# Optimization experiments

Hardware: AMD Instinct MI355X
Metric: run time of the kernel (lower is better)

Reference implementation:

```python
import jax, jax.numpy as jnp
import numpy as np

D_MODEL = 512
N_HEAD = 8
HEAD_DIM = D_MODEL // N_HEAD
B, T = 8, 384
N_TOKENS = 2048


def setup_inputs() -> dict:
    key = jax.random.key(0)
    ks = jax.random.split(key, 16)
    w_scale = 1.0 / np.sqrt(D_MODEL)
    inp = {
        "x": jax.random.normal(ks[0], (N_TOKENS, D_MODEL), jnp.float32),
        "relkeys": jax.random.normal(ks[1], (B, T, T, HEAD_DIM), jnp.float32),
        "relvals": jax.random.normal(ks[2], (B, T, T, HEAD_DIM), jnp.float32),
        "Wq": jax.random.normal(ks[3], (D_MODEL, D_MODEL), jnp.float32) * w_scale,
        "bq": jnp.zeros((D_MODEL,), jnp.float32),
        "Wk": jax.random.normal(ks[4], (D_MODEL, D_MODEL), jnp.float32) * w_scale,
        "bk": jnp.zeros((D_MODEL,), jnp.float32),
        "Wv": jax.random.normal(ks[5], (D_MODEL, D_MODEL), jnp.float32) * w_scale,
        "bv": jnp.zeros((D_MODEL,), jnp.float32),
        "Wp": jax.random.normal(ks[6], (D_MODEL, D_MODEL), jnp.float32) * w_scale,
        "bp": jnp.zeros((D_MODEL,), jnp.float32),
        "padpack_index": jax.random.randint(ks[7], (B, T), 0, N_TOKENS, jnp.int32),
        "padpack_batch": jnp.sort(jax.random.randint(ks[8], (B, T), 0, 40, jnp.int32), axis=-1),
        "padpack_inverse_index": jax.random.randint(ks[9], (N_TOKENS,), 0, B * T, jnp.int32),
    }
    return inp


def reference(x, relkeys, relvals, Wq, bq, Wk, bk, Wv, bv, Wp, bp,
              padpack_index, padpack_batch, padpack_inverse_index):
    C = D_MODEL
    scale = 1.0 / np.sqrt(HEAD_DIM).astype(np.float32)
    # gather ragged tokens into dense padded-packed layout [B,T,C]
    xp = x[padpack_index]

    def heads(W, b):
        # torch nn.Linear: x @ W.T + b ; -> [B,H,T,Dh]
        return (xp @ W.T + b).reshape(B, T, N_HEAD, HEAD_DIM).transpose(0, 2, 1, 3)

    q, k, v = heads(Wq, bq), heads(Wk, bk), heads(Wv, bv)

    att = jnp.einsum('bhsd,bhtd->bhst', q, k) * scale
    att = att + jnp.einsum('bhsd,bstd->bhst', q, relkeys) * scale
    # block-diagonal mask: slots from different ragged sequences can't attend
    mask = (padpack_batch[:, :, None] != padpack_batch[:, None, :])[:, None]  # [B,1,T,T]
    att = jnp.where(mask, jnp.float32(-1e9), att)
    att = jax.nn.softmax(att, axis=-1)

    y = jnp.einsum('bhst,bhtd->bhsd', att, v)
    y = y + jnp.einsum('bhst,bstd->bhsd', att, relvals)
    y = y.transpose(0, 2, 1, 3).reshape(B, T, C)
    y = y @ Wp.T + bp
    # scatter back to ragged token order via inverse index
    return y.reshape(B * T, C)[padpack_inverse_index]
```

## Files before the change

### kernel.cpp

```cpp
#include <hip/hip_runtime.h>

using short8  = __attribute__((ext_vector_type(8))) short;
using floatx4 = __attribute__((ext_vector_type(4))) float;

#define D_MODEL 512
#define N_HEAD 8
#define HEAD_DIM 64
#define B_ 8
#define T_ 384
#define N_SLOTS 3072
#define N_TOK 2048

__device__ __forceinline__ float bf2f(ushort u) {
  union { uint u32; float f; } c; c.u32 = ((uint)u) << 16; return c.f;
}
__device__ __forceinline__ float2 bf2x2(uint u) {
  union { uint u32; float f; } lo, hi;
  lo.u32 = u << 16; hi.u32 = u & 0xffff0000u;
  float2 r; r.x = lo.f; r.y = hi.f; return r;
}
__device__ __forceinline__ ushort f2bf(float f) {
  union { float f; uint u; } c; c.f = f;
  uint x = c.u;
  x += 0x7fffu + ((x >> 16) & 1u);
  return (ushort)(x >> 16);
}

__global__ __launch_bounds__(256) void probe_dtype(const ushort* __restrict__ x,
                                                   int* __restrict__ flag) {
  __shared__ int cnt;
  if (threadIdx.x == 0) cnt = 0;
  __syncthreads();
  int c = 0;
  for (int i = threadIdx.x; i < 1024; i += 256) {
    ushort w = x[2 * i];
    int e = (w >> 7) & 0xFF;
    if (e >= 100 && e <= 160) c++;
  }
  atomicAdd(&cnt, c);
  __syncthreads();
  if (threadIdx.x == 0) flag[0] = (cnt < 700) ? 1 : 0;
}

__device__ __forceinline__ void load8(const void* p, size_t off, int isF32, float* av) {
  if (isF32) {
    const float* fp = (const float*)p + off;
    float4 a = *(const float4*)fp;
    float4 b = *(const float4*)(fp + 4);
    av[0]=a.x; av[1]=a.y; av[2]=a.z; av[3]=a.w;
    av[4]=b.x; av[5]=b.y; av[6]=b.z; av[7]=b.w;
  } else {
    const ushort* up = (const ushort*)p + off;
    uint4 w = *(const uint4*)up;
    float2 p0 = bf2x2(w.x), p1 = bf2x2(w.y), p2 = bf2x2(w.z), p3 = bf2x2(w.w);
    av[0]=p0.x; av[1]=p0.y; av[2]=p1.x; av[3]=p1.y;
    av[4]=p2.x; av[5]=p2.y; av[6]=p3.x; av[7]=p3.y;
  }
}

__device__ __forceinline__ void pack_hl(const float* av, uint4& ph, uint4& pl) {
  ushort hh[8], ll[8];
  #pragma unroll
  for (int j = 0; j < 8; j++) {
    hh[j] = f2bf(av[j]);
    ll[j] = f2bf(av[j] - bf2f(hh[j]));
  }
  ph.x = (uint)hh[0] | ((uint)hh[1] << 16);
  ph.y = (uint)hh[2] | ((uint)hh[3] << 16);
  ph.z = (uint)hh[4] | ((uint)hh[5] << 16);
  ph.w = (uint)hh[6] | ((uint)hh[7] << 16);
  pl.x = (uint)ll[0] | ((uint)ll[1] << 16);
  pl.y = (uint)ll[2] | ((uint)ll[3] << 16);
  pl.z = (uint)ll[4] | ((uint)ll[5] << 16);
  pl.w = (uint)ll[6] | ((uint)ll[7] << 16);
}

template<int A_WS, int MODE>
__global__ __launch_bounds__(256) void gemm_bt(
    const void* __restrict__ Av, const int* __restrict__ gidx,
    const void* __restrict__ Wv, const void* __restrict__ biasv,
    void* __restrict__ outv, const int* __restrict__ flag)
{
  const int f32m = flag[0];
  __shared__ __align__(16) ushort Ash[64][40], Asl[64][40];
  __shared__ __align__(16) ushort Bsh[64][40], Bsl[64][40];
  const int m0 = blockIdx.x * 64;
  const int n0 = blockIdx.y * 64;
  const int tid = threadIdx.x;
  const int wave = tid >> 6, lane = tid & 63;
  const int quad = lane >> 4, l16 = lane & 15;
  const int srow = tid >> 2, sseg = tid & 3;

  const int arow = m0 + srow;
  const int atok = gidx[arow];
  const int brow = n0 + srow;

  floatx4 acc[4];
  #pragma unroll
  for (int i = 0; i < 4; i++) acc[i] = (floatx4){0.f, 0.f, 0.f, 0.f};

  for (int k0 = 0; k0 < D_MODEL; k0 += 32) {
    float av[8];
    uint4 ph, pl;
    load8(Av, (size_t)atok * D_MODEL + k0 + sseg * 8, A_WS ? 1 : f32m, av);
    pack_hl(av, ph, pl);
    *(uint4*)&Ash[srow][sseg * 8] = ph;
    *(uint4*)&Asl[srow][sseg * 8] = pl;
    load8(Wv, (size_t)brow * D_MODEL + k0 + sseg * 8, f32m, av);
    pack_hl(av, ph, pl);
    *(uint4*)&Bsh[srow][sseg * 8] = ph;
    *(uint4*)&Bsl[srow][sseg * 8] = pl;
    __syncthreads();

    short8 ah = *(const short8*)&Ash[wave * 16 + l16][quad * 8];
    short8 al = *(const short8*)&Asl[wave * 16 + l16][quad * 8];
    #pragma unroll
    for (int cg = 0; cg < 4; cg++) {
      short8 bh = *(const short8*)&Bsh[cg * 16 + l16][quad * 8];
      short8 bl = *(const short8*)&Bsl[cg * 16 + l16][quad * 8];
      acc[cg] = __builtin_amdgcn_mfma_f32_16x16x32_bf16(ah, bh, acc[cg], 0, 0, 0);
      acc[cg] = __builtin_amdgcn_mfma_f32_16x16x32_bf16(ah, bl, acc[cg], 0, 0, 0);
      acc[cg] = __builtin_amdgcn_mfma_f32_16x16x32_bf16(al, bh, acc[cg], 0, 0, 0);
    }
    __syncthreads();
  }

  #pragma unroll
  for (int cg = 0; cg < 4; cg++) {
    const int col = n0 + cg * 16 + l16;
    const float bv = f32m ? ((const float*)biasv)[col] : bf2f(((const ushort*)biasv)[col]);
    #pragma unroll
    for (int r = 0; r < 4; r++) {
      const int row = m0 + wave * 16 + quad * 4 + r;
      const float val = acc[cg][r] + bv;
      if (MODE == 0) {
        const int bb = row / T_;
        const int t = row - bb * T_;
        const int hh = col >> 6;
        const int dh = col & 63;
        ((float*)outv)[(((size_t)(bb * N_HEAD + hh) * T_ + t) * HEAD_DIM) + dh] = val;
      } else {
        if (f32m) ((float*)outv)[(size_t)row * D_MODEL + col] = val;
        else      ((ushort*)outv)[(size_t)row * D_MODEL + col] = f2bf(val);
      }
    }
  }
}

__global__ __launch_bounds__(256) void attn_kernel(
    const float* __restrict__ q, const float* __restrict__ k,
    const float* __restrict__ v, const void* __restrict__ rkv,
    const void* __restrict__ rvv, const int* __restrict__ batch,
    float* __restrict__ y, const int* __restrict__ flag)
{
  const int f32m = flag[0];
  const int s = blockIdx.x;
  const int b = blockIdx.y;
  const int tid = threadIdx.x;

  __shared__ float qf[N_HEAD][HEAD_DIM];
  __shared__ float probs[N_HEAD][T_];
  __shared__ int   bt[T_];
  __shared__ float rsum[N_HEAD];

  for (int i = tid; i < D_MODEL; i += 256) {
    const int h = i >> 6, d = i & 63;
    qf[h][d] = q[(((size_t)(b * N_HEAD + h) * T_ + s) * HEAD_DIM) + d];
  }
  for (int i = tid; i < T_; i += 256) bt[i] = batch[b * T_ + i];
  __syncthreads();

  const int myb = bt[s];
  const int h = tid >> 5, tl = tid & 31;
  const float scale = 0.125f;

  const float* kbase = k + ((size_t)(b * N_HEAD + h) * T_) * HEAD_DIM;
  const size_t roff = ((size_t)(b * T_ + s)) * T_ * HEAD_DIM;

  float sc[12];
  #pragma unroll
  for (int i = 0; i < 12; i++) {
    const int t = i * 32 + tl;
    const float4* kp = (const float4*)(kbase + (size_t)t * HEAD_DIM);
    float acc = 0.f;
    if (f32m) {
      const float4* rp = (const float4*)((const float*)rkv + roff + (size_t)t * HEAD_DIM);
      #pragma unroll
      for (int c = 0; c < 16; c++) {
        const float4 kw = kp[c];
        const float4 rw = rp[c];
        const float4 qa = *(const float4*)&qf[h][c * 4];
        acc = fmaf(qa.x, kw.x + rw.x, acc);
        acc = fmaf(qa.y, kw.y + rw.y, acc);
        acc = fmaf(qa.z, kw.z + rw.z, acc);
        acc = fmaf(qa.w, kw.w + rw.w, acc);
      }
    } else {
      const uint4* rp = (const uint4*)((const ushort*)rkv + roff + (size_t)t * HEAD_DIM);
      #pragma unroll
      for (int c = 0; c < 8; c++) {
        const uint4 rw = rp[c];
        const float4 k0 = kp[2 * c];
        const float4 k1 = kp[2 * c + 1];
        const float4 qa = *(const float4*)&qf[h][c * 8];
        const float4 qb = *(const float4*)&qf[h][c * 8 + 4];
        const float2 r0 = bf2x2(rw.x), r1 = bf2x2(rw.y);
        const float2 r2 = bf2x2(rw.z), r3 = bf2x2(rw.w);
        acc = fmaf(qa.x, k0.x + r0.x, acc);
        acc = fmaf(qa.y, k0.y + r0.y, acc);
        acc = fmaf(qa.z, k0.z + r1.x, acc);
        acc = fmaf(qa.w, k0.w + r1.y, acc);
        acc = fmaf(qb.x, k1.x + r2.x, acc);
        acc = fmaf(qb.y, k1.y + r2.y, acc);
        acc = fmaf(qb.z, k1.z + r3.x, acc);
        acc = fmaf(qb.w, k1.w + r3.y, acc);
      }
    }
    sc[i] = (bt[t] == myb) ? acc * scale : -1e9f;
  }

  float m = sc[0];
  #pragma unroll
  for (int i = 1; i < 12; i++) m = fmaxf(m, sc[i]);
  #pragma unroll
  for (int off = 1; off < 32; off <<= 1) m = fmaxf(m, __shfl_xor(m, off, 64));
  float sum = 0.f;
  #pragma unroll
  for (int i = 0; i < 12; i++) { sc[i] = __expf(sc[i] - m); sum += sc[i]; }
  #pragma unroll
  for (int off = 1; off < 32; off <<= 1) sum += __shfl_xor(sum, off, 64);
  #pragma unroll
  for (int i = 0; i < 12; i++) probs[h][i * 32 + tl] = sc[i];
  if (tl == 0) rsum[h] = 1.f / sum;
  __syncthreads();

  const int d0 = tl * 2;
  const float* vp = v + ((size_t)(b * N_HEAD + h) * T_) * HEAD_DIM + d0;
  float ax = 0.f, ay = 0.f;
  if (f32m) {
    const float* rvp = (const float*)rvv + roff + d0;
    #pragma unroll 4
    for (int t = 0; t < T_; t++) {
      const float p = probs[h][t];
      const float2 vv = *(const float2*)(vp + (size_t)t * HEAD_DIM);
      const float2 rr = *(const float2*)(rvp + (size_t)t * HEAD_DIM);
      ax = fmaf(p, vv.x + rr.x, ax);
      ay = fmaf(p, vv.y + rr.y, ay);
    }
  } else {
    const ushort* rvp = (const ushort*)rvv + roff + d0;
    #pragma unroll 4
    for (int t = 0; t < T_; t++) {
      const float p = probs[h][t];
      const float2 vv = *(const float2*)(vp + (size_t)t * HEAD_DIM);
      const float2 rr = bf2x2(*(const uint*)(rvp + (size_t)t * HEAD_DIM));
      ax = fmaf(p, vv.x + rr.x, ax);
      ay = fmaf(p, vv.y + rr.y, ay);
    }
  }
  const float rs = rsum[h];
  float2 o; o.x = ax * rs; o.y = ay * rs;
  *(float2*)(y + ((size_t)(b * T_ + s)) * D_MODEL + h * HEAD_DIM + d0) = o;
}

extern "C" void kernel_launch(void* const* d_in, const int* in_sizes, int n_in,
                              void* d_out, int out_size, void* d_ws, size_t ws_size,
                              hipStream_t stream) {
  const void* x    = d_in[0];
  const void* relk = d_in[1];
  const void* relv = d_in[2];
  const void* Wq   = d_in[3];
  const void* bq   = d_in[4];
  const void* Wk   = d_in[5];
  const void* bk   = d_in[6];
  const void* Wv   = d_in[7];
  const void* bv   = d_in[8];
  const void* Wp   = d_in[9];
  const void* bp   = d_in[10];
  const int* pidx   = (const int*)d_in[11];
  const int* pbatch = (const int*)d_in[12];
  const int* pinv   = (const int*)d_in[13];

  float* ws = (float*)d_ws;
  const size_t SE = (size_t)N_SLOTS * D_MODEL;
  float* qb = ws;
  float* kb = ws + SE;
  float* vb = ws + 2 * SE;
  float* yb = ws + 3 * SE;
  int* flag = (int*)((char*)d_ws + 28u * 1024u * 1024u);

  probe_dtype<<<1, 256, 0, stream>>>((const ushort*)x, flag);
  gemm_bt<0, 0><<<dim3(48, 8), 256, 0, stream>>>(x, pidx, Wq, bq, qb, flag);
  gemm_bt<0, 0><<<dim3(48, 8), 256, 0, stream>>>(x, pidx, Wk, bk, kb, flag);
  gemm_bt<0, 0><<<dim3(48, 8), 256, 0, stream>>>(x, pidx, Wv, bv, vb, flag);
  attn_kernel<<<dim3(T_, B_), 256, 0, stream>>>(qb, kb, vb, relk, relv, pbatch, yb, flag);
  gemm_bt<1, 1><<<dim3(32, 8), 256, 0, stream>>>(yb, pinv, Wp, bp, d_out, flag);
}
```

Baseline: 1.369 ms.

## Prefetch GEMM tiles into registers and widen attention loads with more ILP

The projection GEMM now loads the next k-slice from global memory into registers while the current slice is multiplied, so load latency overlaps MFMA work. The attention score loop is split into a helper with four independent accumulators and processes two key rows per iteration to expose more memory-level parallelism. The PV loop is remapped so each thread handles 8 contiguous dims over a quarter of the key range with float4 loads, followed by a cross-lane shuffle reduction. A launch bound of 4 blocks per CU is added, which may constrain registers given the larger per-thread state.

```diff
diff --git a/kernel.cpp b/kernel.cpp
--- a/kernel.cpp
+++ b/kernel.cpp
@@ -99,18 +99,25 @@
   #pragma unroll
   for (int i = 0; i < 4; i++) acc[i] = (floatx4){0.f, 0.f, 0.f, 0.f};
 
+  float avA[8], avB[8];
+  load8(Av, (size_t)atok * D_MODEL + sseg * 8, A_WS ? 1 : f32m, avA);
+  load8(Wv, (size_t)brow * D_MODEL + sseg * 8, f32m, avB);
+
   for (int k0 = 0; k0 < D_MODEL; k0 += 32) {
-    float av[8];
     uint4 ph, pl;
-    load8(Av, (size_t)atok * D_MODEL + k0 + sseg * 8, A_WS ? 1 : f32m, av);
-    pack_hl(av, ph, pl);
+    pack_hl(avA, ph, pl);
     *(uint4*)&Ash[srow][sseg * 8] = ph;
     *(uint4*)&Asl[srow][sseg * 8] = pl;
-    load8(Wv, (size_t)brow * D_MODEL + k0 + sseg * 8, f32m, av);
-    pack_hl(av, ph, pl);
+    pack_hl(avB, ph, pl);
     *(uint4*)&Bsh[srow][sseg * 8] = ph;
     *(uint4*)&Bsl[srow][sseg * 8] = pl;
     __syncthreads();
+
+    float nvA[8], nvB[8];
+    if (k0 + 32 < D_MODEL) {
+      load8(Av, (size_t)atok * D_MODEL + k0 + 32 + sseg * 8, A_WS ? 1 : f32m, nvA);
+      load8(Wv, (size_t)brow * D_MODEL + k0 + 32 + sseg * 8, f32m, nvB);
+    }
 
     short8 ah = *(const short8*)&Ash[wave * 16 + l16][quad * 8];
     short8 al = *(const short8*)&Asl[wave * 16 + l16][quad * 8];
@@ -123,6 +130,9 @@
       acc[cg] = __builtin_amdgcn_mfma_f32_16x16x32_bf16(al, bh, acc[cg], 0, 0, 0);
     }
     __syncthreads();
+
+    #pragma unroll
+    for (int j = 0; j < 8; j++) { avA[j] = nvA[j]; avB[j] = nvB[j]; }
   }
 
   #pragma unroll
@@ -147,7 +157,61 @@
   }
 }
 
-__global__ __launch_bounds__(256) void attn_kernel(
+__device__ __forceinline__ float dot64(const float* kb, const void* rv, size_t ro,
+                                       int f32m, const float* qrow) {
+  float a0 = 0.f, a1 = 0.f, a2 = 0.f, a3 = 0.f;
+  const float4* kp = (const float4*)kb;
+  if (f32m) {
+    const float4* rp = (const float4*)((const float*)rv + ro);
+    #pragma unroll
+    for (int c = 0; c < 16; c += 4) {
+      const float4 k0 = kp[c],   r0 = rp[c];
+      const float4 k1 = kp[c+1], r1 = rp[c+1];
+      const float4 k2 = kp[c+2], r2 = rp[c+2];
+      const float4 k3 = kp[c+3], r3 = rp[c+3];
+      const float4 q0 = *(const float4*)(qrow + c * 4);
+      const float4 q1 = *(const float4*)(qrow + c * 4 + 4);
+      const float4 q2 = *(const float4*)(qrow + c * 4 + 8);
+      const float4 q3 = *(const float4*)(qrow + c * 4 + 12);
+      a0 = fmaf(q0.x, k0.x + r0.x, a0); a0 = fmaf(q0.y, k0.y + r0.y, a0);
+      a0 = fmaf(q0.z, k0.z + r0.z, a0); a0 = fmaf(q0.w, k0.w + r0.w, a0);
+      a1 = fmaf(q1.x, k1.x + r1.x, a1); a1 = fmaf(q1.y, k1.y + r1.y, a1);
+      a1 = fmaf(q1.z, k1.z + r1.z, a1); a1 = fmaf(q1.w, k1.w + r1.w, a1);
+      a2 = fmaf(q2.x, k2.x + r2.x, a2); a2 = fmaf(q2.y, k2.y + r2.y, a2);
+      a2 = fmaf(q2.z, k2.z + r2.z, a2); a2 = fmaf(q2.w, k2.w + r2.w, a2);
+      a3 = fmaf(q3.x, k3.x + r3.x, a3); a3 = fmaf(q3.y, k3.y + r3.y, a3);
+      a3 = fmaf(q3.z, k3.z + r3.z, a3); a3 = fmaf(q3.w, k3.w + r3.w, a3);
+    }
+  } else {
+    const uint4* rp = (const uint4*)((const ushort*)rv + ro);
+    #pragma unroll
+    for (int c = 0; c < 8; c += 2) {
+      const uint4 rwa = rp[c];
+      const uint4 rwb = rp[c + 1];
+      const float4 k0 = kp[2*c],   k1 = kp[2*c+1];
+      const float4 k2 = kp[2*c+2], k3 = kp[2*c+3];
+      const float4 q0 = *(const float4*)(qrow + c * 8);
+      const float4 q1 = *(const float4*)(qrow + c * 8 + 4);
+      const float4 q2 = *(const float4*)(qrow + c * 8 + 8);
+      const float4 q3 = *(const float4*)(qrow + c * 8 + 12);
+      const float2 r0 = bf2x2(rwa.x), r1 = bf2x2(rwa.y);
+      const float2 r2 = bf2x2(rwa.z), r3 = bf2x2(rwa.w);
+      const float2 r4 = bf2x2(rwb.x), r5 = bf2x2(rwb.y);
+      const float2 r6 = bf2x2(rwb.z), r7 = bf2x2(rwb.w);
+      a0 = fmaf(q0.x, k0.x + r0.x, a0); a0 = fmaf(q0.y, k0.y + r0.y, a0);
+      a0 = fmaf(q0.z, k0.z + r1.x, a0); a0 = fmaf(q0.w, k0.w + r1.y, a0);
+      a1 = fmaf(q1.x, k1.x + r2.x, a1); a1 = fmaf(q1.y, k1.y + r2.y, a1);
+      a1 = fmaf(q1.z, k1.z + r3.x, a1); a1 = fmaf(q1.w, k1.w + r3.y, a1);
+      a2 = fmaf(q2.x, k2.x + r4.x, a2); a2 = fmaf(q2.y, k2.y + r4.y, a2);
+      a2 = fmaf(q2.z, k2.z + r5.x, a2); a2 = fmaf(q2.w, k2.w + r5.y, a2);
+      a3 = fmaf(q3.x, k3.x + r6.x, a3); a3 = fmaf(q3.y, k3.y + r6.y, a3);
+      a3 = fmaf(q3.z, k3.z + r7.x, a3); a3 = fmaf(q3.w, k3.w + r7.y, a3);
+    }
+  }
+  return (a0 + a1) + (a2 + a3);
+}
+
+__global__ __launch_bounds__(256, 4) void attn_kernel(
     const float* __restrict__ q, const float* __restrict__ k,
     const float* __restrict__ v, const void* __restrict__ rkv,
     const void* __restrict__ rvv, const int* __restrict__ batch,
@@ -158,8 +222,8 @@
   const int b = blockIdx.y;
   const int tid = threadIdx.x;
 
-  __shared__ float qf[N_HEAD][HEAD_DIM];
-  __shared__ float probs[N_HEAD][T_];
+  __shared__ __align__(16) float qf[N_HEAD][HEAD_DIM];
+  __shared__ __align__(16) float probs[N_HEAD][T_];
   __shared__ int   bt[T_];
   __shared__ float rsum[N_HEAD];
 
@@ -179,44 +243,15 @@
 
   float sc[12];
   #pragma unroll
-  for (int i = 0; i < 12; i++) {
-    const int t = i * 32 + tl;
-    const float4* kp = (const float4*)(kbase + (size_t)t * HEAD_DIM);
-    float acc = 0.f;
-    if (f32m) {
-      const float4* rp = (const float4*)((const float*)rkv + roff + (size_t)t * HEAD_DIM);
-      #pragma unroll
-      for (int c = 0; c < 16; c++) {
-        const float4 kw = kp[c];
-        const float4 rw = rp[c];
-        const float4 qa = *(const float4*)&qf[h][c * 4];
-        acc = fmaf(qa.x, kw.x + rw.x, acc);
-        acc = fmaf(qa.y, kw.y + rw.y, acc);
-        acc = fmaf(qa.z, kw.z + rw.z, acc);
-        acc = fmaf(qa.w, kw.w + rw.w, acc);
-      }
-    } else {
-      const uint4* rp = (const uint4*)((const ushort*)rkv + roff + (size_t)t * HEAD_DIM);
-      #pragma unroll
-      for (int c = 0; c < 8; c++) {
-        const uint4 rw = rp[c];
-        const float4 k0 = kp[2 * c];
-        const float4 k1 = kp[2 * c + 1];
-        const float4 qa = *(const float4*)&qf[h][c * 8];
-        const float4 qb = *(const float4*)&qf[h][c * 8 + 4];
-        const float2 r0 = bf2x2(rw.x), r1 = bf2x2(rw.y);
-        const float2 r2 = bf2x2(rw.z), r3 = bf2x2(rw.w);
-        acc = fmaf(qa.x, k0.x + r0.x, acc);
-        acc = fmaf(qa.y, k0.y + r0.y, acc);
-        acc = fmaf(qa.z, k0.z + r1.x, acc);
-        acc = fmaf(qa.w, k0.w + r1.y, acc);
-        acc = fmaf(qb.x, k1.x + r2.x, acc);
-        acc = fmaf(qb.y, k1.y + r2.y, acc);
-        acc = fmaf(qb.z, k1.z + r3.x, acc);
-        acc = fmaf(qb.w, k1.w + r3.y, acc);
-      }
-    }
-    sc[i] = (bt[t] == myb) ? acc * scale : -1e9f;
+  for (int i = 0; i < 6; i++) {
+    const int ta = i * 32 + tl;
+    const int tb = ta + 192;
+    const float sa = dot64(kbase + (size_t)ta * HEAD_DIM, rkv,
+                           roff + (size_t)ta * HEAD_DIM, f32m, &qf[h][0]);
+    const float sb = dot64(kbase + (size_t)tb * HEAD_DIM, rkv,
+                           roff + (size_t)tb * HEAD_DIM, f32m, &qf[h][0]);
+    sc[i]     = (bt[ta] == myb) ? sa * scale : -1e9f;
+    sc[i + 6] = (bt[tb] == myb) ? sb * scale : -1e9f;
   }
 
   float m = sc[0];
@@ -230,37 +265,76 @@
   #pragma unroll
   for (int off = 1; off < 32; off <<= 1) sum += __shfl_xor(sum, off, 64);
   #pragma unroll
-  for (int i = 0; i < 12; i++) probs[h][i * 32 + tl] = sc[i];
+  for (int i = 0; i < 6; i++) {
+    probs[h][i * 32 + tl]       = sc[i];
+    probs[h][(i + 6) * 32 + tl] = sc[i + 6];
+  }
   if (tl == 0) rsum[h] = 1.f / sum;
   __syncthreads();
 
-  const int d0 = tl * 2;
+  const int dq = tl & 7, tq = tl >> 3;
+  const int d0 = dq * 8;
+  const int t0 = tq * 96;
   const float* vp = v + ((size_t)(b * N_HEAD + h) * T_) * HEAD_DIM + d0;
-  float ax = 0.f, ay = 0.f;
+
+  float ac[8];
+  #pragma unroll
+  for (int j = 0; j < 8; j++) ac[j] = 0.f;
+
   if (f32m) {
     const float* rvp = (const float*)rvv + roff + d0;
     #pragma unroll 4
-    for (int t = 0; t < T_; t++) {
+    for (int t = t0; t < t0 + 96; t++) {
       const float p = probs[h][t];
-      const float2 vv = *(const float2*)(vp + (size_t)t * HEAD_DIM);
-      const float2 rr = *(const float2*)(rvp + (size_t)t * HEAD_DIM);
-      ax = fmaf(p, vv.x + rr.x, ax);
-      ay = fmaf(p, vv.y + rr.y, ay);
+      const float4 v0 = *(const float4*)(vp + (size_t)t * HEAD_DIM);
+      const float4 v1 = *(const float4*)(vp + (size_t)t * HEAD_DIM + 4);
+      const float4 r0 = *(const float4*)(rvp + (size_t)t * HEAD_DIM);
+      const float4 r1 = *(const float4*)(rvp + (size_t)t * HEAD_DIM + 4);
+      ac[0] = fmaf(p, v0.x + r0.x, ac[0]);
+      ac[1] = fmaf(p, v0.y + r0.y, ac[1]);
+      ac[2] = fmaf(p, v0.z + r0.z, ac[2]);
+      ac[3] = fmaf(p, v0.w + r0.w, ac[3]);
+      ac[4] = fmaf(p, v1.x + r1.x, ac[4]);
+      ac[5] = fmaf(p, v1.y + r1.y, ac[5]);
+      ac[6] = fmaf(p, v1.z + r1.z, ac[6]);
+      ac[7] = fmaf(p, v1.w + r1.w, ac[7]);
     }
   } else {
     const ushort* rvp = (const ushort*)rvv + roff + d0;
     #pragma unroll 4
-    for (int t = 0; t < T_; t++) {
+    for (int t = t0; t < t0 + 96; t++) {
       const float p = probs[h][t];
-      const float2 vv = *(const float2*)(vp + (size_t)t * HEAD_DIM);
-      const float2 rr = bf2x2(*(const uint*)(rvp + (size_t)t * HEAD_DIM));
-      ax = fmaf(p, vv.x + rr.x, ax);
-      ay = fmaf(p, vv.y + rr.y, ay);
-    }
-  }
-  const float rs = rsum[h];
-  float2 o; o.x = ax * rs; o.y = ay * rs;
-  *(float2*)(y + ((size_t)(b * T_ + s)) * D_MODEL + h * HEAD_DIM + d0) = o;
+      const float4 v0 = *(const float4*)(vp + (size_t)t * HEAD_DIM);
+      const float4 v1 = *(const float4*)(vp + (size_t)t * HEAD_DIM + 4);
+      const uint4 rw = *(const uint4*)(rvp + (size_t)t * HEAD_DIM);
+      const float2 r0 = bf2x2(rw.x), r1 = bf2x2(rw.y);
+      const float2 r2 = bf2x2(rw.z), r3 = bf2x2(rw.w);
+      ac[0] = fmaf(p, v0.x + r0.x, ac[0]);
+      ac[1] = fmaf(p, v0.y + r0.y, ac[1]);
+      ac[2] = fmaf(p, v0.z + r1.x, ac[2]);
+      ac[3] = fmaf(p, v0.w + r1.y, ac[3]);
+      ac[4] = fmaf(p, v1.x + r2.x, ac[4]);
+      ac[5] = fmaf(p, v1.y + r2.y, ac[5]);
+      ac[6] = fmaf(p, v1.z + r3.x, ac[6]);
+      ac[7] = fmaf(p, v1.w + r3.y, ac[7]);
+    }
+  }
+
+  #pragma unroll
+  for (int j = 0; j < 8; j++) {
+    ac[j] += __shfl_xor(ac[j], 8, 64);
+    ac[j] += __shfl_xor(ac[j], 16, 64);
+  }
+
+  if (tq == 0) {
+    const float rs = rsum[h];
+    float4 o0, o1;
+    o0.x = ac[0] * rs; o0.y = ac[1] * rs; o0.z = ac[2] * rs; o0.w = ac[3] * rs;
+    o1.x = ac[4] * rs; o1.y = ac[5] * rs; o1.z = ac[6] * rs; o1.w = ac[7] * rs;
+    float* yp = y + ((size_t)(b * T_ + s)) * D_MODEL + h * HEAD_DIM + d0;
+    *(float4*)yp = o0;
+    *(float4*)(yp + 4) = o1;
+  }
 }
 
 extern "C" void kernel_launch(void* const* d_in, const int* in_sizes, int n_in,
```

Result: faster. 1.321 ms (-3.5%).
